# Kernel tuning notes

Hardware: AMD Instinct MI355X
Metric: run time of the kernel (lower is better)

The kernel has to match this reference:

```python
import jax, jax.numpy as jnp
import numpy as np

B, N, DIN, DOUT = 4, 4096, 128, 64
SCALE = float(DOUT)  # scale defaults to out_features


def setup_inputs() -> dict:
    key = jax.random.key(0)
    kx, kq, kk, kv = jax.random.split(key, 4)
    x = jax.random.normal(kx, (B, N, DIN), dtype=jnp.float32)
    # nn.Linear weights, stored as [in, out] so projection is x @ W
    Wq = jax.random.normal(kq, (DIN, DOUT), dtype=jnp.float32) * 0.02
    Wk = jax.random.normal(kk, (DIN, DOUT), dtype=jnp.float32) * 0.02
    Wv = jax.random.normal(kv, (DIN, DOUT), dtype=jnp.float32) * 0.02
    return {"x": x, "Wq": Wq, "Wk": Wk, "Wv": Wv}


def reference(x, Wq, Wk, Wv):
    # Projections: [B, N, DOUT]
    q = jnp.einsum("bnd,de->bne", x, Wq)
    k = jnp.einsum("bnd,de->bne", x, Wk)
    v = jnp.einsum("bnd,de->bne", x, Wv)
    # torch.cdist(q, k, p=2): Euclidean distance matrix [B, N, N]
    q_sq = jnp.sum(q * q, axis=-1)  # [B, N]
    k_sq = jnp.sum(k * k, axis=-1)  # [B, N]
    d2 = q_sq[:, :, None] + k_sq[:, None, :] - 2.0 * jnp.einsum("bne,bme->bnm", q, k)
    dist = jnp.sqrt(jnp.maximum(d2, 0.0))  # clamp for numerical safety
    att = jax.nn.softmax(dist / jnp.sqrt(jnp.float32(SCALE)), axis=-1)
    return jnp.einsum("bnm,bme->bne", att, v)
```

## Files before the change

kernel.cpp:

```cpp
#include <hip/hip_runtime.h>
#include <cstdint>
#include <cstddef>

#define B_ 4
#define N_ 4096
#define DIN_ 128

#define C2_ 0.0325213905f
#define NEG2C2_ (-0.0650427810f)

typedef __attribute__((ext_vector_type(8))) short short8;
typedef __attribute__((ext_vector_type(4))) float f32x4;
typedef __attribute__((ext_vector_type(4))) unsigned short us4;
typedef __attribute__((ext_vector_type(4))) unsigned int u32x4;

#if defined(__has_builtin)
#if __has_builtin(__builtin_amdgcn_exp2f)
#define EXP2(x) __builtin_amdgcn_exp2f(x)
#else
#define EXP2(x) exp2f(x)
#endif
#else
#define EXP2(x) exp2f(x)
#endif

__device__ __forceinline__ unsigned short f2bf(float f) {
    union { float f; unsigned int i; } v; v.f = f;
    unsigned int i = v.i;
    return (unsigned short)((i + 0x7FFFu + ((i >> 16) & 1u)) >> 16);
}

__device__ __forceinline__ unsigned int cvt_pk_bf16(float lo, float hi) {
    unsigned int r;
    asm("v_cvt_pk_bf16_f32 %0, %1, %2" : "=v"(r) : "v"(lo), "v"(hi));
    return r;
}

__global__ __launch_bounds__(256, 2) void proj_kernel(
    const float* __restrict__ x, const float* __restrict__ Wq,
    const float* __restrict__ Wk, const float* __restrict__ Wv,
    unsigned short* __restrict__ qb, unsigned short* __restrict__ kb,
    unsigned short* __restrict__ vT, float* __restrict__ qsq,
    float* __restrict__ ksq)
{
    __shared__ __align__(16) char smem[16384 + 3 * 16384];
    char* xb = smem;

    const int t = threadIdx.x;
    const int R0 = blockIdx.x * 64;

#pragma unroll
    for (int j = 0; j < 8; ++j) {
        const int i = t + 256 * j;
        const int row = i >> 5, c4 = i & 31;
        const float4 v = *(const float4*)(x + (size_t)(R0 + row) * DIN_ + c4 * 4);
        uint2 p2;
        p2.x = cvt_pk_bf16(v.x, v.y);
        p2.y = cvt_pk_bf16(v.z, v.w);
        *(uint2*)(xb + ((row * 256 + c4 * 8) ^ ((row & 7) << 4))) = p2;
    }

    {
        const int c = t & 63, dg = t >> 6;
        const int sw = (c & 7) << 4;
#pragma unroll
        for (int p = 0; p < 3; ++p) {
            const float* __restrict__ Wp = (p == 0) ? Wq : ((p == 1) ? Wk : Wv);
            char* wTp = smem + 16384 + p * 16384;
            float wv[32];
#pragma unroll
            for (int d = 0; d < 32; ++d)
                wv[d] = Wp[(size_t)(dg * 32 + d) * 64 + c];
            unsigned int pk[16];
#pragma unroll
            for (int i = 0; i < 16; ++i) pk[i] = cvt_pk_bf16(wv[2 * i], wv[2 * i + 1]);
#pragma unroll
            for (int q16 = 0; q16 < 4; ++q16)
                *(uint4*)(wTp + ((c * 256 + dg * 64 + q16 * 16) ^ sw)) =
                    *(const uint4*)&pk[q16 * 4];
        }
    }
    __syncthreads();

    const int w = t >> 6, lane = t & 63, li = lane & 15, g = lane >> 4;

    short8 xa[4];
    {
        const int ar = w * 16 + li;
        const int swa = (ar & 7) << 4;
#pragma unroll
        for (int s = 0; s < 4; ++s)
            xa[s] = *(const short8*)(xb + ((ar * 256 + s * 64 + g * 16) ^ swa));
    }

    f32x4 acc[3][4];
#pragma unroll
    for (int p = 0; p < 3; ++p)
#pragma unroll
        for (int c2 = 0; c2 < 4; ++c2) acc[p][c2] = (f32x4){0.f, 0.f, 0.f, 0.f};

#pragma unroll
    for (int p = 0; p < 3; ++p) {
        char* wTp = smem + 16384 + p * 16384;
#pragma unroll
        for (int c2 = 0; c2 < 4; ++c2) {
            const int br = c2 * 16 + li;
            const int swb = (br & 7) << 4;
#pragma unroll
            for (int s = 0; s < 4; ++s) {
                const short8 wb = *(const short8*)(wTp + ((br * 256 + s * 64 + g * 16) ^ swb));
                acc[p][c2] = __builtin_amdgcn_mfma_f32_16x16x32_bf16(xa[s], wb, acc[p][c2], 0, 0, 0);
            }
        }
    }

    const int rbase = R0 + w * 16 + g * 4;
#pragma unroll
    for (int p = 0; p < 2; ++p) {
        unsigned short* dst = (p == 0) ? qb : kb;
#pragma unroll
        for (int c2 = 0; c2 < 4; ++c2)
#pragma unroll
            for (int r = 0; r < 4; ++r)
                dst[(size_t)(rbase + r) * 64 + c2 * 16 + li] = f2bf(acc[p][c2][r]);
#pragma unroll
        for (int r = 0; r < 4; ++r) {
            float s = 0.f;
#pragma unroll
            for (int c2 = 0; c2 < 4; ++c2)
                s = fmaf(acc[p][c2][r], acc[p][c2][r], s);
            s += __shfl_xor(s, 1);
            s += __shfl_xor(s, 2);
            s += __shfl_xor(s, 4);
            s += __shfl_xor(s, 8);
            if (li == 0) {
                float* sq = (p == 0) ? qsq : ksq;
                sq[rbase + r] = s;
            }
        }
    }
    {
        const int bb = R0 >> 12;
        const int n0 = (R0 & (N_ - 1)) + w * 16 + g * 4;
#pragma unroll
        for (int c2 = 0; c2 < 4; ++c2) {
            us4 pk = { f2bf(acc[2][c2][0]), f2bf(acc[2][c2][1]),
                       f2bf(acc[2][c2][2]), f2bf(acc[2][c2][3]) };
            *(us4*)(vT + ((size_t)bb * 64 + c2 * 16 + li) * N_ + n0) = pk;
        }
    }
}

__global__ __launch_bounds__(256, 4) void attn_kernel(
    const unsigned short* __restrict__ qb, const unsigned short* __restrict__ kb,
    const unsigned short* __restrict__ vT, const float* __restrict__ qsq,
    const float* __restrict__ ksq, float* __restrict__ Opart,
    float* __restrict__ Lpart, int ktn)
{
    __shared__ __align__(16) char smem[8192 * 2 + 256];
    char* Klds = smem;
    char* Vlds = smem + 8192;
    float* ksql = (float*)(smem + 16384);

    const int t = threadIdx.x;
    const int w = t >> 6, lane = t & 63, li = lane & 15, g = lane >> 4;
    const int b = blockIdx.y, sp = blockIdx.z;
    const int q0 = blockIdx.x * 128;
    const int kt0 = sp * ktn;

    const size_t qbase = ((size_t)b * N_ + q0 + w * 32) * 64;
    short8 qa[2][2];
    float qsc[2];
#pragma unroll
    for (int h = 0; h < 2; ++h) {
        qa[h][0] = *(const short8*)(qb + qbase + (size_t)(h * 16 + li) * 64 + g * 8);
        qa[h][1] = *(const short8*)(qb + qbase + (size_t)(h * 16 + li) * 64 + 32 + g * 8);
        qsc[h] = qsq[(size_t)b * N_ + q0 + w * 32 + h * 16 + li] * C2_;
    }

    f32x4 oa[2][4];
    float lsum[2];
#pragma unroll
    for (int h = 0; h < 2; ++h) {
        lsum[h] = 0.f;
#pragma unroll
        for (int i = 0; i < 4; ++i) oa[h][i] = (f32x4){0.f, 0.f, 0.f, 0.f};
    }

    const unsigned short* kbb = kb + (size_t)b * N_ * 64;
    const unsigned short* vtb = vT + (size_t)b * 64 * N_;
    const float* ksqb = ksq + (size_t)b * N_;

    const int row0 = t >> 3, cc0 = t & 7;
    const int row1 = row0 + 32;
    const int lb0 = (row0 * 128 + cc0 * 16) ^ ((row0 & 7) << 4);
    const int lb1 = (row1 * 128 + cc0 * 16) ^ ((row1 & 7) << 4);

    const int krbase = ((li >> 2) << 3) + (li & 3);

    for (int ktl = 0; ktl < ktn; ++ktl) {
        const int kt = kt0 + ktl;
        *(uint4*)(Klds + lb0) = *(const uint4*)(kbb + (size_t)(kt * 64 + row0) * 64 + cc0 * 8);
        *(uint4*)(Klds + lb1) = *(const uint4*)(kbb + (size_t)(kt * 64 + row1) * 64 + cc0 * 8);
        *(uint4*)(Vlds + lb0) = *(const uint4*)(vtb + (size_t)row0 * N_ + kt * 64 + cc0 * 8);
        *(uint4*)(Vlds + lb1) = *(const uint4*)(vtb + (size_t)row1 * N_ + kt * 64 + cc0 * 8);
        if (t < 64) ksql[t] = ksqb[kt * 64 + t] * C2_;
        __syncthreads();

        u32x4 pa0[2], pa1[2];
#pragma unroll
        for (int c = 0; c < 4; ++c) {
            const int koff = ((c & 1) << 2) + ((c >> 1) << 5);
            const int kr = krbase + koff;
            const int sw = (kr & 7) << 4;
            const short8 kf0 = *(const short8*)(Klds + ((kr * 128 + g * 16) ^ sw));
            const short8 kf1 = *(const short8*)(Klds + ((kr * 128 + 64 + g * 16) ^ sw));
            f32x4 s[2];
            __builtin_amdgcn_s_setprio(1);
#pragma unroll
            for (int h = 0; h < 2; ++h) {
                s[h] = (f32x4){0.f, 0.f, 0.f, 0.f};
                s[h] = __builtin_amdgcn_mfma_f32_16x16x32_bf16(kf0, qa[h][0], s[h], 0, 0, 0);
                s[h] = __builtin_amdgcn_mfma_f32_16x16x32_bf16(kf1, qa[h][1], s[h], 0, 0, 0);
            }
            __builtin_amdgcn_s_setprio(0);

            const float4 ksc = *(const float4*)(ksql + 8 * g + koff);
            const float kscv[4] = { ksc.x, ksc.y, ksc.z, ksc.w };
#pragma unroll
            for (int h = 0; h < 2; ++h) {
                float p[4];
#pragma unroll
                for (int r = 0; r < 4; ++r) {
                    const float d2 = fmaf(NEG2C2_, s[h][r], qsc[h] + kscv[r]);
                    const float ds = __builtin_amdgcn_sqrtf(fmaxf(d2, 0.0f));
                    p[r] = EXP2(ds);
                    lsum[h] += p[r];
                }
                const unsigned int lo = cvt_pk_bf16(p[0], p[1]);
                const unsigned int hi = cvt_pk_bf16(p[2], p[3]);
                if (c == 0)      { pa0[h].x = lo; pa0[h].y = hi; }
                else if (c == 1) { pa0[h].z = lo; pa0[h].w = hi; }
                else if (c == 2) { pa1[h].x = lo; pa1[h].y = hi; }
                else             { pa1[h].z = lo; pa1[h].w = hi; }
            }
        }

        short8 paf[2][2];
#pragma unroll
        for (int h = 0; h < 2; ++h) {
            paf[h][0] = __builtin_bit_cast(short8, pa0[h]);
            paf[h][1] = __builtin_bit_cast(short8, pa1[h]);
        }
        __builtin_amdgcn_s_setprio(1);
#pragma unroll
        for (int c2 = 0; c2 < 4; ++c2) {
            const int er = c2 * 16 + li;
            const int swv = (er & 7) << 4;
            const short8 vf0 = *(const short8*)(Vlds + ((er * 128 + g * 16) ^ swv));
            const short8 vf1 = *(const short8*)(Vlds + ((er * 128 + 64 + g * 16) ^ swv));
#pragma unroll
            for (int h = 0; h < 2; ++h) {
                oa[h][c2] = __builtin_amdgcn_mfma_f32_16x16x32_bf16(paf[h][0], vf0, oa[h][c2], 0, 0, 0);
                oa[h][c2] = __builtin_amdgcn_mfma_f32_16x16x32_bf16(paf[h][1], vf1, oa[h][c2], 0, 0, 0);
            }
        }
        __builtin_amdgcn_s_setprio(0);
        __syncthreads();
    }

    const size_t obase = ((size_t)sp * B_ + b) * N_;
#pragma unroll
    for (int h = 0; h < 2; ++h) {
        float ls = lsum[h];
        ls += __shfl_xor(ls, 16);
        ls += __shfl_xor(ls, 32);
        if (lane < 16) Lpart[obase + q0 + w * 32 + h * 16 + li] = ls;
#pragma unroll
        for (int c2 = 0; c2 < 4; ++c2)
#pragma unroll
            for (int r = 0; r < 4; ++r)
                Opart[(obase + q0 + w * 32 + h * 16 + g * 4 + r) * 64 + c2 * 16 + li]
                    = oa[h][c2][r];
    }
}

__global__ __launch_bounds__(256) void reduce_kernel(
    const float* __restrict__ Opart, const float* __restrict__ Lpart,
    float* __restrict__ out, int S)
{
    const int idx = blockIdx.x * 256 + threadIdx.x;
    const int rowg = idx >> 4;
    const int e4 = (idx & 15) << 2;
    float l = 0.f;
    float4 o = {0.f, 0.f, 0.f, 0.f};
    for (int s = 0; s < S; ++s) {
        l += Lpart[(size_t)s * (B_ * N_) + rowg];
        const float4 v = *(const float4*)(Opart + ((size_t)s * (B_ * N_) + rowg) * 64 + e4);
        o.x += v.x; o.y += v.y; o.z += v.z; o.w += v.w;
    }
    const float inv = 1.0f / l;
    const float4 res = {o.x * inv, o.y * inv, o.z * inv, o.w * inv};
    *(float4*)(out + (size_t)rowg * 64 + e4) = res;
}

extern "C" void kernel_launch(void* const* d_in, const int* in_sizes, int n_in,
                              void* d_out, int out_size, void* d_ws, size_t ws_size,
                              hipStream_t stream) {
    (void)in_sizes; (void)n_in; (void)out_size;
    const float* x  = (const float*)d_in[0];
    const float* Wq = (const float*)d_in[1];
    const float* Wk = (const float*)d_in[2];
    const float* Wv = (const float*)d_in[3];

    char* ws = (char*)d_ws;
    const size_t MB = 1024 * 1024;
    unsigned short* qb = (unsigned short*)(ws);
    unsigned short* kb = (unsigned short*)(ws + 2 * MB);
    unsigned short* vT = (unsigned short*)(ws + 4 * MB);
    float* qsq = (float*)(ws + 6 * MB);
    float* ksq = (float*)(ws + 6 * MB + 65536);
    float* Lpart = (float*)(ws + 6 * MB + 262144);

    int S;
    float* Opart;
    if (ws_size >= 7 * MB + 32 * MB)      { S = 8; Opart = (float*)(ws + 7 * MB); }
    else if (ws_size >= 7 * MB + 16 * MB) { S = 4; Opart = (float*)(ws + 7 * MB); }
    else if (ws_size >= 7 * MB + 8 * MB)  { S = 2; Opart = (float*)(ws + 7 * MB); }
    else if (ws_size >= 7 * MB + 4 * MB)  { S = 1; Opart = (float*)(ws + 7 * MB); }
    else                                  { S = 1; Opart = (float*)d_out; }

    hipLaunchKernelGGL(proj_kernel, dim3(256), dim3(256), 0, stream,
                       x, Wq, Wk, Wv, qb, kb, vT, qsq, ksq);
    hipLaunchKernelGGL(attn_kernel, dim3(32, B_, S), dim3(256), 0, stream,
                       qb, kb, vT, qsq, ksq, Opart, Lpart, 64 / S);
    hipLaunchKernelGGL(reduce_kernel, dim3(1024), dim3(256), 0, stream,
                       Opart, Lpart, (float*)d_out, S);
}
```

Measured before the change: 53.03 us.

## Double-buffer K/V tiles in attention using direct global-to-LDS loads

The attention loop now stages the next K and V tiles into a second LDS buffer with global_load_lds while the current tile is computed, and prefetches the key squared norms through a register. This drops one barrier per iteration and overlaps global-memory latency with MFMA and softmax work. LDS use doubles to about 33 KB per block, which may limit occupancy at four blocks per CU. Correctness depends on global_load_lds placing each lane's 16 bytes in the matching swizzled LDS slot.

```diff
diff --git a/kernel.cpp b/kernel.cpp
--- a/kernel.cpp
+++ b/kernel.cpp
@@ -36,6 +36,12 @@
     return r;
 }
 
+__device__ __forceinline__ void gload16(const void* g, void* l) {
+    __builtin_amdgcn_global_load_lds(
+        (const __attribute__((address_space(1))) void*)g,
+        (__attribute__((address_space(3))) void*)l, 16, 0, 0);
+}
+
 __global__ __launch_bounds__(256, 2) void proj_kernel(
     const float* __restrict__ x, const float* __restrict__ Wq,
     const float* __restrict__ Wk, const float* __restrict__ Wv,
@@ -157,10 +163,8 @@
     const float* __restrict__ ksq, float* __restrict__ Opart,
     float* __restrict__ Lpart, int ktn)
 {
-    __shared__ __align__(16) char smem[8192 * 2 + 256];
-    char* Klds = smem;
-    char* Vlds = smem + 8192;
-    float* ksql = (float*)(smem + 16384);
+    __shared__ __align__(16) char smem[32768 + 512];
+    float* ksql = (float*)(smem + 32768);
 
     const int t = threadIdx.x;
     const int w = t >> 6, lane = t & 63, li = lane & 15, g = lane >> 4;
@@ -191,21 +195,40 @@
     const unsigned short* vtb = vT + (size_t)b * 64 * N_;
     const float* ksqb = ksq + (size_t)b * N_;
 
-    const int row0 = t >> 3, cc0 = t & 7;
-    const int row1 = row0 + 32;
-    const int lb0 = (row0 * 128 + cc0 * 16) ^ ((row0 & 7) << 4);
-    const int lb1 = (row1 * 128 + cc0 * 16) ^ ((row1 & 7) << 4);
+    const int lrow = lane >> 3;
+    const int lcc = (lane & 7) ^ lrow;
+
+#define STAGE(bufi, kt)                                                          \
+    {                                                                            \
+        _Pragma("unroll")                                                        \
+        for (int jj = 0; jj < 2; ++jj) {                                         \
+            const int j = 2 * w + jj;                                            \
+            const int row = 8 * j + lrow;                                        \
+            gload16(kbb + (size_t)((kt) * 64 + row) * 64 + lcc * 8,              \
+                    smem + (bufi) * 8192 + j * 1024);                            \
+            gload16(vtb + (size_t)row * N_ + (kt) * 64 + lcc * 8,                \
+                    smem + 16384 + (bufi) * 8192 + j * 1024);                    \
+        }                                                                        \
+    }
 
     const int krbase = ((li >> 2) << 3) + (li & 3);
 
+    STAGE(0, kt0);
+    if (t < 64) ksql[t] = ksqb[kt0 * 64 + t] * C2_;
+    __syncthreads();
+
+    int buf = 0;
     for (int ktl = 0; ktl < ktn; ++ktl) {
-        const int kt = kt0 + ktl;
-        *(uint4*)(Klds + lb0) = *(const uint4*)(kbb + (size_t)(kt * 64 + row0) * 64 + cc0 * 8);
-        *(uint4*)(Klds + lb1) = *(const uint4*)(kbb + (size_t)(kt * 64 + row1) * 64 + cc0 * 8);
-        *(uint4*)(Vlds + lb0) = *(const uint4*)(vtb + (size_t)row0 * N_ + kt * 64 + cc0 * 8);
-        *(uint4*)(Vlds + lb1) = *(const uint4*)(vtb + (size_t)row1 * N_ + kt * 64 + cc0 * 8);
-        if (t < 64) ksql[t] = ksqb[kt * 64 + t] * C2_;
-        __syncthreads();
+        const bool more = (ktl + 1 < ktn);
+        float ksn = 0.f;
+        if (more) {
+            STAGE(buf ^ 1, kt0 + ktl + 1);
+            if (t < 64) ksn = ksqb[(kt0 + ktl + 1) * 64 + t] * C2_;
+        }
+
+        char* Klds = smem + buf * 8192;
+        char* Vlds = smem + 16384 + buf * 8192;
+        const float* ksqlb = ksql + buf * 64;
 
         u32x4 pa0[2], pa1[2];
 #pragma unroll
@@ -225,7 +248,7 @@
             }
             __builtin_amdgcn_s_setprio(0);
 
-            const float4 ksc = *(const float4*)(ksql + 8 * g + koff);
+            const float4 ksc = *(const float4*)(ksqlb + 8 * g + koff);
             const float kscv[4] = { ksc.x, ksc.y, ksc.z, ksc.w };
 #pragma unroll
             for (int h = 0; h < 2; ++h) {
@@ -266,8 +289,12 @@
             }
         }
         __builtin_amdgcn_s_setprio(0);
+
+        if (more && t < 64) ksql[(buf ^ 1) * 64 + t] = ksn;
         __syncthreads();
-    }
+        buf ^= 1;
+    }
+#undef STAGE
 
     const size_t obase = ((size_t)sp * B_ + b) * N_;
 #pragma unroll
```

Result: slower. 61.90 us (+16.7%).
